# Kernel optimization log

Measured on AMD Instinct MI355X. Metric: run time of the kernel, lower is better.

## Reference

```python
import jax, jax.numpy as jnp
import numpy as np

H, D, E, S_E, P_E, N, B = 16, 48, 768, 384, 128, 768, 1

def _ln(x, g=None, b=None, eps=1e-5):
    mu = jnp.mean(x, axis=-1, keepdims=True)
    var = jnp.var(x, axis=-1, keepdims=True)
    y = (x - mu) * jax.lax.rsqrt(var + eps)
    if g is not None:
        y = y * g
    if b is not None:
        y = y + b
    return y

def setup_inputs() -> dict:
    key = jax.random.key(0)
    ks = jax.random.split(key, 16)
    sc_e = 1.0 / np.sqrt(E)
    sc_s = 1.0 / np.sqrt(S_E)
    sc_p = 1.0 / np.sqrt(P_E)
    return {
        "a": jax.random.normal(ks[0], (B, N, E), jnp.float32),
        "s": jax.random.normal(ks[1], (B, N, S_E), jnp.float32),
        "pair_rep": jax.random.normal(ks[2], (B, N, N, P_E), jnp.float32),
        "beta": jax.random.normal(ks[3], (B, N, N), jnp.float32),
        # AdaLN: sigmoid-gated scale and shift from s
        "w_ada_gamma": jax.random.normal(ks[4], (S_E, E), jnp.float32) * sc_s,
        "w_ada_beta": jax.random.normal(ks[5], (S_E, E), jnp.float32) * sc_s,
        # q/k/v projections, stored as [E, H, D]
        "wq": jax.random.normal(ks[6], (E, H, D), jnp.float32) * sc_e,
        "bq": jnp.zeros((H, D), jnp.float32),
        "wk": jax.random.normal(ks[7], (E, H, D), jnp.float32) * sc_e,
        "wv": jax.random.normal(ks[8], (E, H, D), jnp.float32) * sc_e,
        # pair bias: LayerNorm(P_E) + Linear(P_E -> H, no bias)
        "ln_pair_g": jnp.ones((P_E,), jnp.float32),
        "ln_pair_b": jnp.zeros((P_E,), jnp.float32),
        "w_pair": jax.random.normal(ks[9], (P_E, H), jnp.float32) * sc_p,
        # gate projection [E, H, D], no bias, sigmoid
        "w_gate": jax.random.normal(ks[10], (E, H, D), jnp.float32) * sc_e,
        # output projections
        "w_proj_a": jax.random.normal(ks[11], (E, E), jnp.float32) * sc_e,
        "w_out": jax.random.normal(ks[12], (S_E, E), jnp.float32) * sc_s,
        "b_out": jnp.full((E,), -2.0, jnp.float32),
    }

def reference(a, s, pair_rep, beta, w_ada_gamma, w_ada_beta, wq, bq, wk, wv,
              ln_pair_g, ln_pair_b, w_pair, w_gate, w_proj_a, w_out, b_out):
    # AdaLN: normalize a (no affine); gamma/beta conditioned on normalized s
    a_n = _ln(a)
    s_n = _ln(s)
    gamma = jax.nn.sigmoid(s_n @ w_ada_gamma)
    a_mod = gamma * a_n + s_n @ w_ada_beta            # [B,N,E]

    q = jnp.einsum('bne,ehd->bnhd', a_mod, wq) + bq   # [B,N,H,D]
    k = jnp.einsum('bne,ehd->bnhd', a_mod, wk)
    v = jnp.einsum('bne,ehd->bnhd', a_mod, wv)
    g = jax.nn.sigmoid(jnp.einsum('bne,ehd->bnhd', a_mod, w_gate))

    # per-head pair bias: LN(pair) @ w_pair + beta -> [B,H,N,N]
    b = jnp.einsum('bnmp,ph->bhnm', _ln(pair_rep, ln_pair_g, ln_pair_b), w_pair)
    b = b + beta[:, None, :, :]

    scale = 1.0 / np.sqrt(D)
    logits = jnp.einsum('bnhd,bmhd->bhnm', q, k) * scale + b
    weights = jax.nn.softmax(logits, axis=-1)         # [B,H,N,N]

    attn = jnp.einsum('bhnm,bmhd->bhnd', weights, v)
    attn = attn * jnp.moveaxis(g, -2, -3)             # gate per head
    attn = jnp.moveaxis(attn, -3, -2).reshape(a.shape[0], a.shape[1], H * D)
    out = attn @ w_proj_a                             # [B,N,E]
    out = jax.nn.sigmoid(s @ w_out + b_out) * out
    return out
```

## Files before the change

kernel.cpp:

```cpp
#include <hip/hip_runtime.h>
#include <hip/hip_bf16.h>

typedef __attribute__((ext_vector_type(8))) short short8;
typedef __attribute__((ext_vector_type(8))) unsigned short u16x8;
typedef __attribute__((ext_vector_type(4))) unsigned short u16x4;
typedef __attribute__((ext_vector_type(4))) float f32x4;
typedef __attribute__((ext_vector_type(4))) unsigned u32x4;

#define NTOK 768
#define ED   768
#define SD   384
#define PD   128
#define NH   16
#define DH   48
#define LGS  778

__device__ __forceinline__ unsigned short f2bf(float x) {
  unsigned u = __builtin_bit_cast(unsigned, x);
  u += 0x7FFFu + ((u >> 16) & 1u);
  return (unsigned short)(u >> 16);
}
__device__ __forceinline__ float bf2f(unsigned short b) {
  unsigned u = ((unsigned)b) << 16;
  return __builtin_bit_cast(float, u);
}
__device__ __forceinline__ float sigm(float x) { return 1.0f / (1.0f + __expf(-x)); }

__device__ __forceinline__ unsigned cvtpk(float a, float b) {
  unsigned r;
  asm("v_cvt_pk_bf16_f32 %0, %1, %2" : "=v"(r) : "v"(a), "v"(b));
  return r;
}
__device__ __forceinline__ float lo2f(unsigned p) {
  return __builtin_bit_cast(float, p << 16);
}
__device__ __forceinline__ float hi2f(unsigned p) {
  return __builtin_bit_cast(float, p & 0xFFFF0000u);
}

__device__ __forceinline__ void gl2lds(const unsigned short* g, unsigned short* l) {
  __builtin_amdgcn_global_load_lds(
      (const __attribute__((address_space(1))) unsigned int*)g,
      (__attribute__((address_space(3))) unsigned int*)l, 16, 0, 0);
}

constexpr size_t SZ_SN   = (size_t)NTOK * SD * 2;
constexpr size_t OFF_SNH = 0;
constexpr size_t OFF_SNL = OFF_SNH + SZ_SN;
constexpr size_t OFF_SRH = OFF_SNL + SZ_SN;
constexpr size_t OFF_SRL = OFF_SRH + SZ_SN;
constexpr size_t OFF_GAM = OFF_SRL + SZ_SN;
constexpr size_t OFF_BET = OFF_GAM + 2359296;
constexpr size_t OFF_OG  = OFF_BET + 2359296;
constexpr size_t OFF_AMH = OFF_OG  + 2359296;
constexpr size_t OFF_AML = OFF_AMH + 1179648;
constexpr size_t OFF_QB  = OFF_AML + 1179648;
constexpr size_t OFF_KB  = OFF_QB  + 1179648;
constexpr size_t OFF_VT  = OFF_KB  + 1179648;
constexpr size_t OFF_GBUF= OFF_VT  + 1179648;
constexpr size_t OFF_AGH = OFF_GBUF+ 2359296;
constexpr size_t OFF_AGL = OFF_AGH + 1179648;
constexpr size_t OFF_WSMH= OFF_AGL + 1179648;
constexpr size_t OFF_WSML= OFF_WSMH+ 1769472;
constexpr size_t OFF_WQH = OFF_WSML+ 1769472;
constexpr size_t OFF_WQL = OFF_WQH + 4718592;
constexpr size_t OFF_WPH = OFF_WQL + 4718592;
constexpr size_t OFF_WPL = OFF_WPH + 1179648;
constexpr size_t OFF_GWH = OFF_WPL + 1179648;
constexpr size_t OFF_GWL = OFF_GWH + 4096;
constexpr size_t OFF_SGW = OFF_GWL + 4096;
constexpr size_t OFF_QKL = OFF_SGW + 4096;
constexpr size_t OFF_PB  = OFF_QKL + 37748736;
constexpr size_t WS_NEED = OFF_PB  + 18874368;

__global__ __launch_bounds__(256) void k_wcvt(
    const float* __restrict__ wag, const float* __restrict__ wab, const float* __restrict__ wo,
    const float* __restrict__ wq, const float* __restrict__ wk, const float* __restrict__ wv,
    const float* __restrict__ wg, const float* __restrict__ wp,
    const float* __restrict__ lng, const float* __restrict__ lnb,
    const float* __restrict__ wpair, const float* __restrict__ s,
    unsigned short* __restrict__ wsmh, unsigned short* __restrict__ wsml,
    unsigned short* __restrict__ wqh, unsigned short* __restrict__ wql,
    unsigned short* __restrict__ wph, unsigned short* __restrict__ wpl,
    unsigned short* __restrict__ gwh, unsigned short* __restrict__ gwl,
    float* __restrict__ sgw, float* __restrict__ bw,
    unsigned short* __restrict__ snh, unsigned short* __restrict__ snl,
    unsigned short* __restrict__ srh, unsigned short* __restrict__ srl) {
  const int tid = threadIdx.x;
  if (blockIdx.z == 8) {
    const int gid = blockIdx.y * 24 + blockIdx.x;
    if (gid == 192) {
      if (tid < 128) {
        float g = lng[tid];
        for (int hh = 0; hh < 16; ++hh) {
          float gwv = g * wpair[tid * 16 + hh];
          unsigned short hb = f2bf(gwv);
          gwh[tid * 16 + hh] = hb;
          gwl[tid * 16 + hh] = f2bf(gwv - bf2f(hb));
        }
      }
      if (tid < 16) {
        float sv = 0.f, bb = 0.f;
        for (int p = 0; p < 128; ++p) {
          float w = wpair[p * 16 + tid];
          sv += lng[p] * w;
          bb += lnb[p] * w;
        }
        sgw[tid] = sv;
        bw[tid]  = bb;
      }
      return;
    }
    if (gid > 192) return;
    const int n = gid * 4 + (tid >> 6);
    const int lane = tid & 63;
    const float* row = s + (size_t)n * SD;
    float v[6], sum = 0.f, sq = 0.f;
#pragma unroll
    for (int i = 0; i < 6; ++i) { v[i] = row[lane + 64 * i]; sum += v[i]; sq += v[i] * v[i]; }
#pragma unroll
    for (int off = 1; off < 64; off <<= 1) { sum += __shfl_xor(sum, off); sq += __shfl_xor(sq, off); }
    float mu = sum * (1.f / SD);
    float var = sq * (1.f / SD) - mu * mu;
    float rs = rsqrtf(var + 1e-5f);
#pragma unroll
    for (int i = 0; i < 6; ++i) {
      size_t idx = (size_t)n * SD + lane + 64 * i;
      float x = v[i];
      unsigned short xh = f2bf(x);
      srh[idx] = xh; srl[idx] = f2bf(x - bf2f(xh));
      float y = (x - mu) * rs;
      unsigned short yh = f2bf(y);
      snh[idx] = yh; snl[idx] = f2bf(y - bf2f(yh));
    }
    return;
  }
  const int id = blockIdx.z;
  const float* src; int Ksrc; unsigned short *dh, *dl; int n0; int Kd;
  switch (id) {
    case 0: src = wag; Ksrc = 384; dh = wsmh; dl = wsml; n0 = 0;    Kd = 384; break;
    case 1: src = wab; Ksrc = 384; dh = wsmh; dl = wsml; n0 = 768;  Kd = 384; break;
    case 2: src = wo;  Ksrc = 384; dh = wsmh; dl = wsml; n0 = 1536; Kd = 384; break;
    case 3: src = wq;  Ksrc = 768; dh = wqh;  dl = wql;  n0 = 0;    Kd = 768; break;
    case 4: src = wk;  Ksrc = 768; dh = wqh;  dl = wql;  n0 = 768;  Kd = 768; break;
    case 5: src = wv;  Ksrc = 768; dh = wqh;  dl = wql;  n0 = 1536; Kd = 768; break;
    case 6: src = wg;  Ksrc = 768; dh = wqh;  dl = wql;  n0 = 2304; Kd = 768; break;
    default: src = wp; Ksrc = 768; dh = wph;  dl = wpl;  n0 = 0;    Kd = 768; break;
  }
  const int kt = blockIdx.x, ntile = blockIdx.y;
  if (kt * 32 >= Ksrc) return;
  __shared__ float t[32][33];
  const int r = tid >> 3, c4 = (tid & 7) * 4;
  float4 v = *(const float4*)(src + (size_t)(kt * 32 + r) * 768 + ntile * 32 + c4);
  t[r][c4 + 0] = v.x; t[r][c4 + 1] = v.y; t[r][c4 + 2] = v.z; t[r][c4 + 3] = v.w;
  __syncthreads();
  u16x4 hv, lv;
#pragma unroll
  for (int j = 0; j < 4; ++j) {
    float x = t[c4 + j][r];
    unsigned short hb = f2bf(x);
    hv[j] = hb;
    lv[j] = f2bf(x - bf2f(hb));
  }
  size_t drow = (size_t)(n0 + ntile * 32 + r) * Kd + kt * 32 + c4;
  *(u16x4*)(dh + drow) = hv;
  *(u16x4*)(dl + drow) = lv;
}

__device__ __forceinline__ void mfma_core(
    const unsigned short* __restrict__ Ah, const unsigned short* __restrict__ Al,
    const unsigned short* __restrict__ Bh, const unsigned short* __restrict__ Bl,
    int K, int mBase, int nBase, f32x4 acc[2][2]) {
  __shared__ unsigned short lds[2][4][4096];
  const int tid = threadIdx.x;
  const int w = tid >> 6, lane = tid & 63;
  const int l15 = lane & 15, kg = lane >> 4;
  const int wr = w >> 1, wc = w & 1;

  size_t offA[2], offB[2];
  int ldsw[2];
#pragma unroll
  for (int i = 0; i < 2; ++i) {
    int chunk = w * 128 + i * 64 + lane;
    int row = chunk >> 3;
    int slot = (chunk & 7) ^ (row & 7);
    offA[i] = (size_t)(mBase + row) * K + slot * 8;
    offB[i] = (size_t)(nBase + row) * K + slot * 8;
    ldsw[i] = w * 1024 + i * 512;
  }
  auto stage = [&](int b, int k0) {
#pragma unroll
    for (int i = 0; i < 2; ++i) {
      gl2lds(Ah + offA[i] + k0, &lds[b][0][ldsw[i]]);
      gl2lds(Al + offA[i] + k0, &lds[b][1][ldsw[i]]);
      gl2lds(Bh + offB[i] + k0, &lds[b][2][ldsw[i]]);
      gl2lds(Bl + offB[i] + k0, &lds[b][3][ldsw[i]]);
    }
  };

  stage(0, 0);
  int buf = 0;
  for (int k0 = 64; k0 <= K; k0 += 64) {
    __syncthreads();
    if (k0 < K) stage(buf ^ 1, k0);
#pragma unroll
    for (int kk = 0; kk < 2; ++kk) {
      short8 ah[2], al[2], bh4[2], bl4[2];
#pragma unroll
      for (int mi = 0; mi < 2; ++mi) {
        int row = wr * 32 + mi * 16 + l15;
        int kb = kk * 64 + kg * 16;
        int idx = row * 64 + ((kb ^ ((row & 7) << 4)) >> 1);
        ah[mi] = *(const short8*)&lds[buf][0][idx];
        al[mi] = *(const short8*)&lds[buf][1][idx];
      }
#pragma unroll
      for (int ni = 0; ni < 2; ++ni) {
        int row = wc * 32 + ni * 16 + l15;
        int kb = kk * 64 + kg * 16;
        int idx = row * 64 + ((kb ^ ((row & 7) << 4)) >> 1);
        bh4[ni] = *(const short8*)&lds[buf][2][idx];
        bl4[ni] = *(const short8*)&lds[buf][3][idx];
      }
#pragma unroll
      for (int mi = 0; mi < 2; ++mi)
#pragma unroll
        for (int ni = 0; ni < 2; ++ni) {
          acc[mi][ni] = __builtin_amdgcn_mfma_f32_16x16x32_bf16(ah[mi], bh4[ni], acc[mi][ni], 0, 0, 0);
          acc[mi][ni] = __builtin_amdgcn_mfma_f32_16x16x32_bf16(al[mi], bh4[ni], acc[mi][ni], 0, 0, 0);
          acc[mi][ni] = __builtin_amdgcn_mfma_f32_16x16x32_bf16(ah[mi], bl4[ni], acc[mi][ni], 0, 0, 0);
        }
    }
    buf ^= 1;
  }
}

__global__ __launch_bounds__(256) void k_gemm_small(
    const unsigned short* __restrict__ snh, const unsigned short* __restrict__ snl,
    const unsigned short* __restrict__ srh, const unsigned short* __restrict__ srl,
    const unsigned short* __restrict__ wsmh, const unsigned short* __restrict__ wsml,
    const float* __restrict__ bo,
    float* __restrict__ gaml, float* __restrict__ betl, float* __restrict__ og) {
  const int nt = blockIdx.x, mt = blockIdx.y;
  const unsigned short* Ah = (nt < 24) ? snh : srh;
  const unsigned short* Al = (nt < 24) ? snl : srl;
  f32x4 acc[2][2];
#pragma unroll
  for (int i = 0; i < 2; ++i)
#pragma unroll
    for (int j = 0; j < 2; ++j) acc[i][j] = (f32x4){0.f, 0.f, 0.f, 0.f};
  mfma_core(Ah, Al, wsmh, wsml, SD, mt * 64, nt * 64, acc);
  const int tid = threadIdx.x;
  const int w = tid >> 6, lane = tid & 63;
  const int l15 = lane & 15, kg = lane >> 4;
  const int wr = w >> 1, wc = w & 1;
#pragma unroll
  for (int mi = 0; mi < 2; ++mi)
#pragma unroll
    for (int ni = 0; ni < 2; ++ni) {
      int col = nt * 64 + wc * 32 + ni * 16 + l15;
#pragma unroll
      for (int r = 0; r < 4; ++r) {
        int row = mt * 64 + wr * 32 + mi * 16 + kg * 4 + r;
        float v = acc[mi][ni][r];
        if (col < 768) gaml[(size_t)row * ED + col] = v;
        else if (col < 1536) betl[(size_t)row * ED + col - 768] = v;
        else og[(size_t)row * ED + col - 1536] = sigm(v + bo[col - 1536]);
      }
    }
}

__global__ __launch_bounds__(256) void k_gemm_qkvg(
    const unsigned short* __restrict__ amh, const unsigned short* __restrict__ aml,
    const unsigned short* __restrict__ wqh, const unsigned short* __restrict__ wql,
    const float* __restrict__ bq,
    unsigned short* __restrict__ qb, unsigned short* __restrict__ kb,
    unsigned short* __restrict__ vT, float* __restrict__ gbuf) {
  const int nt = blockIdx.x, mt = blockIdx.y;
  f32x4 acc[2][2];
#pragma unroll
  for (int i = 0; i < 2; ++i)
#pragma unroll
    for (int j = 0; j < 2; ++j) acc[i][j] = (f32x4){0.f, 0.f, 0.f, 0.f};
  mfma_core(amh, aml, wqh, wql, ED, mt * 64, nt * 64, acc);
  const int tid = threadIdx.x;
  const int w = tid >> 6, lane = tid & 63;
  const int l15 = lane & 15, kg = lane >> 4;
  const int wr = w >> 1, wc = w & 1;
  const int sel = nt / 12;
#pragma unroll
  for (int mi = 0; mi < 2; ++mi)
#pragma unroll
    for (int ni = 0; ni < 2; ++ni) {
      int col = nt * 64 + wc * 32 + ni * 16 + l15;
      int c = col - sel * 768;
#pragma unroll
      for (int r = 0; r < 4; ++r) {
        int row = mt * 64 + wr * 32 + mi * 16 + kg * 4 + r;
        float v = acc[mi][ni][r];
        size_t idx = (size_t)row * ED + c;
        if (sel == 0) qb[idx] = f2bf(v + bq[c]);
        else if (sel == 1) kb[idx] = f2bf(v);
        else if (sel == 2) vT[(size_t)c * NTOK + row] = f2bf(v);
        else gbuf[idx] = sigm(v);
      }
    }
}

__global__ __launch_bounds__(256) void k_gemm_proj(
    const unsigned short* __restrict__ agh, const unsigned short* __restrict__ agl,
    const unsigned short* __restrict__ wph, const unsigned short* __restrict__ wpl,
    const float* __restrict__ og, float* __restrict__ out) {
  const int nt = blockIdx.x, mt = blockIdx.y;
  f32x4 acc[2][2];
#pragma unroll
  for (int i = 0; i < 2; ++i)
#pragma unroll
    for (int j = 0; j < 2; ++j) acc[i][j] = (f32x4){0.f, 0.f, 0.f, 0.f};
  mfma_core(agh, agl, wph, wpl, ED, mt * 64, nt * 64, acc);
  const int tid = threadIdx.x;
  const int w = tid >> 6, lane = tid & 63;
  const int l15 = lane & 15, kg = lane >> 4;
  const int wr = w >> 1, wc = w & 1;
#pragma unroll
  for (int mi = 0; mi < 2; ++mi)
#pragma unroll
    for (int ni = 0; ni < 2; ++ni) {
      int col = nt * 64 + wc * 32 + ni * 16 + l15;
#pragma unroll
      for (int r = 0; r < 4; ++r) {
        int row = mt * 64 + wr * 32 + mi * 16 + kg * 4 + r;
        size_t idx = (size_t)row * ED + col;
        out[idx] = acc[mi][ni][r] * og[idx];
      }
    }
}

__global__ __launch_bounds__(256) void k_amod(const float* __restrict__ a,
                                              const float* __restrict__ gamma_lin,
                                              const float* __restrict__ beta_lin,
                                              unsigned short* __restrict__ amh,
                                              unsigned short* __restrict__ aml) {
  __shared__ float red[8];
  const int n = blockIdx.x, tid = threadIdx.x;
  const int lane = tid & 63, wid = tid >> 6;
  const float* row = a + (size_t)n * ED;
  float v[3], sum = 0.f, sq = 0.f;
#pragma unroll
  for (int i = 0; i < 3; ++i) { v[i] = row[tid + 256 * i]; sum += v[i]; sq += v[i] * v[i]; }
#pragma unroll
  for (int off = 1; off < 64; off <<= 1) { sum += __shfl_xor(sum, off); sq += __shfl_xor(sq, off); }
  if (lane == 0) { red[wid] = sum; red[4 + wid] = sq; }
  __syncthreads();
  float S = red[0] + red[1] + red[2] + red[3];
  float Q = red[4] + red[5] + red[6] + red[7];
  float mu = S * (1.f / ED);
  float var = Q * (1.f / ED) - mu * mu;
  float rs = rsqrtf(var + 1e-5f);
#pragma unroll
  for (int i = 0; i < 3; ++i) {
    int e = tid + 256 * i;
    float an = (v[i] - mu) * rs;
    size_t idx = (size_t)n * ED + e;
    float val = sigm(gamma_lin[idx]) * an + beta_lin[idx];
    unsigned short h = f2bf(val);
    amh[idx] = h;
    aml[idx] = f2bf(val - bf2f(h));
  }
}

__global__ __launch_bounds__(256) void k_qkw(const unsigned short* __restrict__ qb,
                                             const unsigned short* __restrict__ kb,
                                             const float* __restrict__ beta,
                                             float* __restrict__ qkl) {
  const int mt = blockIdx.x, ntile = blockIdx.y, h = blockIdx.z;
  __shared__ unsigned short qs[64 * 72];
  __shared__ unsigned short ksm[64 * 72];
  const int tid = threadIdx.x;
  const int n0 = ntile * 64, m0 = mt * 64;
  const u16x8 z = {0, 0, 0, 0, 0, 0, 0, 0};
#pragma unroll
  for (int it = 0; it < 2; ++it) {
    int idx = tid + it * 256;
    int row = idx >> 3, c = idx & 7;
    u16x8 vq = z, vk = z;
    if (c < 6) {
      vq = *(const u16x8*)(qb + (size_t)(n0 + row) * ED + h * DH + c * 8);
      vk = *(const u16x8*)(kb + (size_t)(m0 + row) * ED + h * DH + c * 8);
    }
    *(u16x8*)(qs + row * 72 + c * 8) = vq;
    *(u16x8*)(ksm + row * 72 + c * 8) = vk;
  }
  __syncthreads();
  const int wv = tid >> 6, lane = tid & 63;
  const int l15 = lane & 15, kg = lane >> 4;
  f32x4 acc[4];
#pragma unroll
  for (int ct = 0; ct < 4; ++ct) acc[ct] = (f32x4){0.f, 0.f, 0.f, 0.f};
#pragma unroll
  for (int ks2 = 0; ks2 < 2; ++ks2) {
    short8 av = *(const short8*)(qs + (wv * 16 + l15) * 72 + ks2 * 32 + kg * 8);
#pragma unroll
    for (int ct = 0; ct < 4; ++ct) {
      short8 bv = *(const short8*)(ksm + (ct * 16 + l15) * 72 + ks2 * 32 + kg * 8);
      acc[ct] = __builtin_amdgcn_mfma_f32_16x16x32_bf16(av, bv, acc[ct], 0, 0, 0);
    }
  }
  const float scale = 0.14433756729740643f;
#pragma unroll
  for (int ct = 0; ct < 4; ++ct)
#pragma unroll
    for (int r = 0; r < 4; ++r) {
      int nn = n0 + wv * 16 + kg * 4 + r;
      int mm = m0 + ct * 16 + l15;
      qkl[((size_t)nn * NH + h) * NTOK + mm] =
          fmaf(acc[ct][r], scale, beta[(size_t)nn * NTOK + mm]);
    }
}

__global__ __launch_bounds__(256, 3) void k_pairsm(const float* __restrict__ pair_rep,
                                                   const float* __restrict__ qkl,
                                                   const unsigned short* __restrict__ gw_hi,
                                                   const unsigned short* __restrict__ gw_lo,
                                                   const float* __restrict__ sgw, const float* __restrict__ bw,
                                                   unsigned short* __restrict__ pb) {
  __shared__ float lg[16 * LGS];
  const int n = blockIdx.x;
  const int tid = threadIdx.x;
  const int wv = tid >> 6, lane = tid & 63;
  const int l15 = lane & 15, kg = lane >> 4;

#define LOADCH(X, CH) do {                                                        \
    const float* xp_ = pair_rep + ((size_t)n * NTOK + (CH) * 16 + l15) * PD + kg * 8; \
    _Pragma("unroll")                                                             \
    for (int q_ = 0; q_ < 4; ++q_) {                                              \
      X[q_ * 2]     = *(const float4*)(xp_ + q_ * 32);                            \
      X[q_ * 2 + 1] = *(const float4*)(xp_ + q_ * 32 + 4);                        \
    }                                                                             \
  } while (0)

  float4 Xa[8], Xb[8];
  LOADCH(Xa, wv);
  LOADCH(Xb, wv + 4);

  short8 bh[4], bl[4];
#pragma unroll
  for (int ks = 0; ks < 4; ++ks)
#pragma unroll
    for (int j = 0; j < 8; ++j) {
      int p = ks * 32 + kg * 8 + j;
      bh[ks][j] = (short)gw_hi[p * 16 + l15];
      bl[ks][j] = (short)gw_lo[p * 16 + l15];
    }
  float sgv[4], bwv[4];
#pragma unroll
  for (int r = 0; r < 4; ++r) { sgv[r] = sgw[kg * 4 + r]; bwv[r] = bw[kg * 4 + r]; }

#define PROC(X, CH) do {                                                          \
    float sum_ = 0.f, sq_ = 0.f;                                                  \
    _Pragma("unroll")                                                             \
    for (int q_ = 0; q_ < 8; ++q_) {                                              \
      sum_ += X[q_].x + X[q_].y + X[q_].z + X[q_].w;                              \
      sq_ = fmaf(X[q_].x, X[q_].x, sq_); sq_ = fmaf(X[q_].y, X[q_].y, sq_);       \
      sq_ = fmaf(X[q_].z, X[q_].z, sq_); sq_ = fmaf(X[q_].w, X[q_].w, sq_);       \
    }                                                                             \
    sum_ += __shfl_xor(sum_, 16); sum_ += __shfl_xor(sum_, 32);                   \
    sq_  += __shfl_xor(sq_, 16);  sq_  += __shfl_xor(sq_, 32);                    \
    float mu_ = sum_ * (1.f / 128.f);                                             \
    float rstd_ = rsqrtf(sq_ * (1.f / 128.f) - mu_ * mu_ + 1e-5f);                \
    f32x4 acc_ = {0.f, 0.f, 0.f, 0.f};                                            \
    _Pragma("unroll")                                                             \
    for (int ks_ = 0; ks_ < 4; ++ks_) {                                           \
      float4 u0_ = X[ks_ * 2], u1_ = X[ks_ * 2 + 1];                              \
      unsigned p0_ = cvtpk(u0_.x, u0_.y), p1_ = cvtpk(u0_.z, u0_.w);              \
      unsigned p2_ = cvtpk(u1_.x, u1_.y), p3_ = cvtpk(u1_.z, u1_.w);              \
      float l0_ = u0_.x - lo2f(p0_), l1_ = u0_.y - hi2f(p0_);                     \
      float l2_ = u0_.z - lo2f(p1_), l3_ = u0_.w - hi2f(p1_);                     \
      float l4_ = u1_.x - lo2f(p2_), l5_ = u1_.y - hi2f(p2_);                     \
      float l6_ = u1_.z - lo2f(p3_), l7_ = u1_.w - hi2f(p3_);                     \
      unsigned q0_ = cvtpk(l0_, l1_), q1_ = cvtpk(l2_, l3_);                      \
      unsigned q2_ = cvtpk(l4_, l5_), q3_ = cvtpk(l6_, l7_);                      \
      u32x4 hp_ = {p0_, p1_, p2_, p3_}, lp_ = {q0_, q1_, q2_, q3_};               \
      short8 ah_ = __builtin_bit_cast(short8, hp_);                               \
      short8 al_ = __builtin_bit_cast(short8, lp_);                               \
      acc_ = __builtin_amdgcn_mfma_f32_16x16x32_bf16(bh[ks_], ah_, acc_, 0, 0, 0);\
      acc_ = __builtin_amdgcn_mfma_f32_16x16x32_bf16(bh[ks_], al_, acc_, 0, 0, 0);\
      acc_ = __builtin_amdgcn_mfma_f32_16x16x32_bf16(bl[ks_], ah_, acc_, 0, 0, 0);\
    }                                                                             \
    _Pragma("unroll")                                                             \
    for (int r_ = 0; r_ < 4; ++r_) {                                              \
      float val_ = rstd_ * (acc_[r_] - mu_ * sgv[r_]) + bwv[r_];                  \
      lg[(kg * 4 + r_) * LGS + (CH) * 16 + l15] = val_;                           \
    }                                                                             \
  } while (0)

  PROC(Xa, wv +  0); LOADCH(Xa, wv +  8);
  PROC(Xb, wv +  4); LOADCH(Xb, wv + 12);
  PROC(Xa, wv +  8); LOADCH(Xa, wv + 16);
  PROC(Xb, wv + 12); LOADCH(Xb, wv + 20);
  PROC(Xa, wv + 16); LOADCH(Xa, wv + 24);
  PROC(Xb, wv + 20); LOADCH(Xb, wv + 28);
  PROC(Xa, wv + 24); LOADCH(Xa, wv + 32);
  PROC(Xb, wv + 28); LOADCH(Xb, wv + 36);
  PROC(Xa, wv + 32); LOADCH(Xa, wv + 40);
  PROC(Xb, wv + 36); LOADCH(Xb, wv + 44);
  PROC(Xa, wv + 40);
  PROC(Xb, wv + 44);
#undef LOADCH
#undef PROC
  __syncthreads();

#pragma unroll
  for (int hh = 0; hh < 4; ++hh) {
    int h = wv * 4 + hh;
    const float* qrow = qkl + ((size_t)n * NH + h) * NTOK;
    float x[12];
#pragma unroll
    for (int i = 0; i < 12; ++i) x[i] = lg[h * LGS + lane + 64 * i] + qrow[lane + 64 * i];
    float mx = x[0];
#pragma unroll
    for (int t = 1; t < 12; ++t) mx = fmaxf(mx, x[t]);
#pragma unroll
    for (int off = 1; off < 64; off <<= 1) mx = fmaxf(mx, __shfl_xor(mx, off));
    float e[12], sm = 0.f;
#pragma unroll
    for (int t = 0; t < 12; ++t) { e[t] = __expf(x[t] - mx); sm += e[t]; }
#pragma unroll
    for (int off = 1; off < 64; off <<= 1) sm += __shfl_xor(sm, off);
    float inv = 1.0f / sm;
    unsigned short* dst = pb + ((size_t)h * NTOK + n) * NTOK;
#pragma unroll
    for (int i = 0; i < 12; ++i) dst[lane + 64 * i] = f2bf(e[i] * inv);
  }
}

__global__ __launch_bounds__(256) void k_pv(const unsigned short* __restrict__ wb,
                                            const unsigned short* __restrict__ vT,
                                            const float* __restrict__ gbuf,
                                            unsigned short* __restrict__ agh,
                                            unsigned short* __restrict__ agl) {
  const int ntile = blockIdx.x, h = blockIdx.y;
  const int n0 = ntile * 64;
  __shared__ unsigned short wsm[2][64 * 40];
  __shared__ unsigned short vtm[2][48 * 40];
  const int tid = threadIdx.x;
  const int wv = tid >> 6, lane = tid & 63, l15 = lane & 15, kg = lane >> 4;
  const int srow = tid >> 2, sc = tid & 3;
  const unsigned short* wsrc = wb + ((size_t)h * NTOK + (n0 + srow)) * NTOK + sc * 8;
  const unsigned short* vsrc = (tid < 192)
      ? vT + (size_t)(h * DH + srow) * NTOK + sc * 8 : nullptr;
  f32x4 acc[3];
#pragma unroll
  for (int dt = 0; dt < 3; ++dt) acc[dt] = (f32x4){0.f, 0.f, 0.f, 0.f};

  *(u16x8*)(wsm[0] + srow * 40 + sc * 8) = *(const u16x8*)(wsrc);
  if (tid < 192)
    *(u16x8*)(vtm[0] + srow * 40 + sc * 8) = *(const u16x8*)(vsrc);
  __syncthreads();

  int buf = 0;
  for (int k0 = 0; k0 < NTOK; k0 += 32) {
    if (k0 + 32 < NTOK) {
      *(u16x8*)(wsm[buf ^ 1] + srow * 40 + sc * 8) = *(const u16x8*)(wsrc + k0 + 32);
      if (tid < 192)
        *(u16x8*)(vtm[buf ^ 1] + srow * 40 + sc * 8) = *(const u16x8*)(vsrc + k0 + 32);
    }
    short8 av = *(const short8*)(wsm[buf] + (wv * 16 + l15) * 40 + kg * 8);
#pragma unroll
    for (int dt = 0; dt < 3; ++dt) {
      short8 bv = *(const short8*)(vtm[buf] + (dt * 16 + l15) * 40 + kg * 8);
      acc[dt] = __builtin_amdgcn_mfma_f32_16x16x32_bf16(av, bv, acc[dt], 0, 0, 0);
    }
    __syncthreads();
    buf ^= 1;
  }
#pragma unroll
  for (int dt = 0; dt < 3; ++dt)
#pragma unroll
    for (int r = 0; r < 4; ++r) {
      int nn = n0 + wv * 16 + kg * 4 + r;
      int col = h * DH + dt * 16 + l15;
      size_t idx = (size_t)nn * ED + col;
      float val = acc[dt][r] * gbuf[idx];
      unsigned short hb = f2bf(val);
      agh[idx] = hb;
      agl[idx] = f2bf(val - bf2f(hb));
    }
}

extern "C" void kernel_launch(void* const* d_in, const int* in_sizes, int n_in,
                              void* d_out, int out_size, void* d_ws, size_t ws_size,
                              hipStream_t stream) {
  const float* a    = (const float*)d_in[0];
  const float* s    = (const float*)d_in[1];
  const float* pair = (const float*)d_in[2];
  const float* beta = (const float*)d_in[3];
  const float* wag  = (const float*)d_in[4];
  const float* wab  = (const float*)d_in[5];
  const float* wq   = (const float*)d_in[6];
  const float* bq   = (const float*)d_in[7];
  const float* wk   = (const float*)d_in[8];
  const float* wvp  = (const float*)d_in[9];
  const float* lng  = (const float*)d_in[10];
  const float* lnb  = (const float*)d_in[11];
  const float* wpair= (const float*)d_in[12];
  const float* wg   = (const float*)d_in[13];
  const float* wproj= (const float*)d_in[14];
  const float* wo   = (const float*)d_in[15];
  const float* bo   = (const float*)d_in[16];
  float* out = (float*)d_out;

  if (ws_size < WS_NEED) return;

  char* ws = (char*)d_ws;
  unsigned short* snh  = (unsigned short*)(ws + OFF_SNH);
  unsigned short* snl  = (unsigned short*)(ws + OFF_SNL);
  unsigned short* srh  = (unsigned short*)(ws + OFF_SRH);
  unsigned short* srl  = (unsigned short*)(ws + OFF_SRL);
  float*          gaml = (float*)(ws + OFF_GAM);
  float*          betl = (float*)(ws + OFF_BET);
  float*          og   = (float*)(ws + OFF_OG);
  unsigned short* amh  = (unsigned short*)(ws + OFF_AMH);
  unsigned short* aml  = (unsigned short*)(ws + OFF_AML);
  unsigned short* qb   = (unsigned short*)(ws + OFF_QB);
  unsigned short* kb   = (unsigned short*)(ws + OFF_KB);
  unsigned short* vT   = (unsigned short*)(ws + OFF_VT);
  float*          gbuf = (float*)(ws + OFF_GBUF);
  unsigned short* agh  = (unsigned short*)(ws + OFF_AGH);
  unsigned short* agl  = (unsigned short*)(ws + OFF_AGL);
  unsigned short* wsmh = (unsigned short*)(ws + OFF_WSMH);
  unsigned short* wsml = (unsigned short*)(ws + OFF_WSML);
  unsigned short* wqh  = (unsigned short*)(ws + OFF_WQH);
  unsigned short* wql  = (unsigned short*)(ws + OFF_WQL);
  unsigned short* wph  = (unsigned short*)(ws + OFF_WPH);
  unsigned short* wpl  = (unsigned short*)(ws + OFF_WPL);
  unsigned short* gwh  = (unsigned short*)(ws + OFF_GWH);
  unsigned short* gwl  = (unsigned short*)(ws + OFF_GWL);
  float*          sgw  = (float*)(ws + OFF_SGW);
  float*          bw   = sgw + 16;
  float*          qkl  = (float*)(ws + OFF_QKL);
  unsigned short* pb   = (unsigned short*)(ws + OFF_PB);

  hipLaunchKernelGGL(k_wcvt, dim3(24, 24, 9), dim3(256), 0, stream,
                     wag, wab, wo, wq, wk, wvp, wg, wproj, lng, lnb, wpair, s,
                     wsmh, wsml, wqh, wql, wph, wpl, gwh, gwl, sgw, bw,
                     snh, snl, srh, srl);
  hipLaunchKernelGGL(k_gemm_small, dim3(36, 12), dim3(256), 0, stream,
                     snh, snl, srh, srl, wsmh, wsml, bo, gaml, betl, og);
  hipLaunchKernelGGL(k_amod, dim3(768), dim3(256), 0, stream, a, gaml, betl, amh, aml);
  hipLaunchKernelGGL(k_gemm_qkvg, dim3(48, 12), dim3(256), 0, stream,
                     amh, aml, wqh, wql, bq, qb, kb, vT, gbuf);
  hipLaunchKernelGGL(k_qkw, dim3(12, 12, 16), dim3(256), 0, stream, qb, kb, beta, qkl);
  hipLaunchKernelGGL(k_pairsm, dim3(768), dim3(256), 0, stream,
                     pair, qkl, gwh, gwl, sgw, bw, pb);
  hipLaunchKernelGGL(k_pv, dim3(12, 16), dim3(256), 0, stream, pb, vT, gbuf, agh, agl);
  hipLaunchKernelGGL(k_gemm_proj, dim3(12, 12), dim3(256), 0, stream,
                     agh, agl, wph, wpl, og, out);
}
```

Baseline: 172.1 us.

## Offload pair-bias LN+projection for first rows into QKVG GEMM launch

Adds 192 extra blocks to the QKVG GEMM grid that compute the layer-normed pair bias for the first 192 query rows and write it to a new global buffer. The pair-softmax kernel then reads the precomputed bias for those rows instead of streaming pair_rep, and computes it inline only for the remaining rows. The aim is to fill idle compute units during the small GEMM and shorten the memory-bound pair kernel. The cost is an extra global round trip of fp32 bias and a larger, more divergent GEMM launch.

```diff
diff --git a/kernel.cpp b/kernel.cpp
--- a/kernel.cpp
+++ b/kernel.cpp
@@ -14,6 +14,7 @@
 #define NH   16
 #define DH   48
 #define LGS  778
+#define NRIDE 192
 
 __device__ __forceinline__ unsigned short f2bf(float x) {
   unsigned u = __builtin_bit_cast(unsigned, x);
@@ -71,7 +72,8 @@
 constexpr size_t OFF_SGW = OFF_GWL + 4096;
 constexpr size_t OFF_QKL = OFF_SGW + 4096;
 constexpr size_t OFF_PB  = OFF_QKL + 37748736;
-constexpr size_t WS_NEED = OFF_PB  + 18874368;
+constexpr size_t OFF_BB  = OFF_PB  + 18874368;
+constexpr size_t WS_NEED = OFF_BB  + 9437184;
 
 __global__ __launch_bounds__(256) void k_wcvt(
     const float* __restrict__ wag, const float* __restrict__ wab, const float* __restrict__ wo,
@@ -167,6 +169,95 @@
   *(u16x4*)(dl + drow) = lv;
 }
 
+__device__ __forceinline__ void pair_bias_rows_to_global(
+    int n, const float* __restrict__ pair_rep,
+    const unsigned short* __restrict__ gw_hi, const unsigned short* __restrict__ gw_lo,
+    const float* __restrict__ sgw, const float* __restrict__ bw,
+    float* __restrict__ bb) {
+  const int tid = threadIdx.x;
+  const int wv = tid >> 6, lane = tid & 63;
+  const int l15 = lane & 15, kg = lane >> 4;
+
+#define LOADCH2(X, CH) do {                                                       \
+    const float* xp_ = pair_rep + ((size_t)n * NTOK + (CH) * 16 + l15) * PD + kg * 8; \
+    _Pragma("unroll")                                                             \
+    for (int q_ = 0; q_ < 4; ++q_) {                                              \
+      X[q_ * 2]     = *(const float4*)(xp_ + q_ * 32);                            \
+      X[q_ * 2 + 1] = *(const float4*)(xp_ + q_ * 32 + 4);                        \
+    }                                                                             \
+  } while (0)
+
+  float4 Xa[8], Xb[8];
+  LOADCH2(Xa, wv);
+  LOADCH2(Xb, wv + 4);
+
+  short8 bh[4], bl[4];
+#pragma unroll
+  for (int ks = 0; ks < 4; ++ks)
+#pragma unroll
+    for (int j = 0; j < 8; ++j) {
+      int p = ks * 32 + kg * 8 + j;
+      bh[ks][j] = (short)gw_hi[p * 16 + l15];
+      bl[ks][j] = (short)gw_lo[p * 16 + l15];
+    }
+  float sgv[4], bwv[4];
+#pragma unroll
+  for (int r = 0; r < 4; ++r) { sgv[r] = sgw[kg * 4 + r]; bwv[r] = bw[kg * 4 + r]; }
+
+#define PROC2(X, CH) do {                                                         \
+    float sum_ = 0.f, sq_ = 0.f;                                                  \
+    _Pragma("unroll")                                                             \
+    for (int q_ = 0; q_ < 8; ++q_) {                                              \
+      sum_ += X[q_].x + X[q_].y + X[q_].z + X[q_].w;                              \
+      sq_ = fmaf(X[q_].x, X[q_].x, sq_); sq_ = fmaf(X[q_].y, X[q_].y, sq_);       \
+      sq_ = fmaf(X[q_].z, X[q_].z, sq_); sq_ = fmaf(X[q_].w, X[q_].w, sq_);       \
+    }                                                                             \
+    sum_ += __shfl_xor(sum_, 16); sum_ += __shfl_xor(sum_, 32);                   \
+    sq_  += __shfl_xor(sq_, 16);  sq_  += __shfl_xor(sq_, 32);                    \
+    float mu_ = sum_ * (1.f / 128.f);                                             \
+    float rstd_ = rsqrtf(sq_ * (1.f / 128.f) - mu_ * mu_ + 1e-5f);                \
+    f32x4 acc_ = {0.f, 0.f, 0.f, 0.f};                                            \
+    _Pragma("unroll")                                                             \
+    for (int ks_ = 0; ks_ < 4; ++ks_) {                                           \
+      float4 u0_ = X[ks_ * 2], u1_ = X[ks_ * 2 + 1];                              \
+      unsigned p0_ = cvtpk(u0_.x, u0_.y), p1_ = cvtpk(u0_.z, u0_.w);              \
+      unsigned p2_ = cvtpk(u1_.x, u1_.y), p3_ = cvtpk(u1_.z, u1_.w);              \
+      float l0_ = u0_.x - lo2f(p0_), l1_ = u0_.y - hi2f(p0_);                     \
+      float l2_ = u0_.z - lo2f(p1_), l3_ = u0_.w - hi2f(p1_);                     \
+      float l4_ = u1_.x - lo2f(p2_), l5_ = u1_.y - hi2f(p2_);                     \
+      float l6_ = u1_.z - lo2f(p3_), l7_ = u1_.w - hi2f(p3_);                     \
+      unsigned q0_ = cvtpk(l0_, l1_), q1_ = cvtpk(l2_, l3_);                      \
+      unsigned q2_ = cvtpk(l4_, l5_), q3_ = cvtpk(l6_, l7_);                      \
+      u32x4 hp_ = {p0_, p1_, p2_, p3_}, lp_ = {q0_, q1_, q2_, q3_};               \
+      short8 ah_ = __builtin_bit_cast(short8, hp_);                               \
+      short8 al_ = __builtin_bit_cast(short8, lp_);                               \
+      acc_ = __builtin_amdgcn_mfma_f32_16x16x32_bf16(bh[ks_], ah_, acc_, 0, 0, 0);\
+      acc_ = __builtin_amdgcn_mfma_f32_16x16x32_bf16(bh[ks_], al_, acc_, 0, 0, 0);\
+      acc_ = __builtin_amdgcn_mfma_f32_16x16x32_bf16(bl[ks_], ah_, acc_, 0, 0, 0);\
+    }                                                                             \
+    _Pragma("unroll")                                                             \
+    for (int r_ = 0; r_ < 4; ++r_) {                                              \
+      float val_ = rstd_ * (acc_[r_] - mu_ * sgv[r_]) + bwv[r_];                  \
+      bb[(size_t)n * (NH * NTOK) + (kg * 4 + r_) * NTOK + (CH) * 16 + l15] = val_;\
+    }                                                                             \
+  } while (0)
+
+  PROC2(Xa, wv +  0); LOADCH2(Xa, wv +  8);
+  PROC2(Xb, wv +  4); LOADCH2(Xb, wv + 12);
+  PROC2(Xa, wv +  8); LOADCH2(Xa, wv + 16);
+  PROC2(Xb, wv + 12); LOADCH2(Xb, wv + 20);
+  PROC2(Xa, wv + 16); LOADCH2(Xa, wv + 24);
+  PROC2(Xb, wv + 20); LOADCH2(Xb, wv + 28);
+  PROC2(Xa, wv + 24); LOADCH2(Xa, wv + 32);
+  PROC2(Xb, wv + 28); LOADCH2(Xb, wv + 36);
+  PROC2(Xa, wv + 32); LOADCH2(Xa, wv + 40);
+  PROC2(Xb, wv + 36); LOADCH2(Xb, wv + 44);
+  PROC2(Xa, wv + 40);
+  PROC2(Xb, wv + 44);
+#undef LOADCH2
+#undef PROC2
+}
+
 __device__ __forceinline__ void mfma_core(
     const unsigned short* __restrict__ Ah, const unsigned short* __restrict__ Al,
     const unsigned short* __restrict__ Bh, const unsigned short* __restrict__ Bl,
@@ -274,9 +365,17 @@
     const unsigned short* __restrict__ amh, const unsigned short* __restrict__ aml,
     const unsigned short* __restrict__ wqh, const unsigned short* __restrict__ wql,
     const float* __restrict__ bq,
+    const float* __restrict__ pair_rep,
+    const unsigned short* __restrict__ gwh, const unsigned short* __restrict__ gwl,
+    const float* __restrict__ sgw, const float* __restrict__ bw,
+    float* __restrict__ biasBuf,
     unsigned short* __restrict__ qb, unsigned short* __restrict__ kb,
     unsigned short* __restrict__ vT, float* __restrict__ gbuf) {
   const int nt = blockIdx.x, mt = blockIdx.y;
+  if (mt >= 12) {
+    pair_bias_rows_to_global((mt - 12) * 48 + nt, pair_rep, gwh, gwl, sgw, bw, biasBuf);
+    return;
+  }
   f32x4 acc[2][2];
 #pragma unroll
   for (int i = 0; i < 2; ++i)
@@ -420,6 +519,7 @@
 
 __global__ __launch_bounds__(256, 3) void k_pairsm(const float* __restrict__ pair_rep,
                                                    const float* __restrict__ qkl,
+                                                   const float* __restrict__ biasBuf,
                                                    const unsigned short* __restrict__ gw_hi,
                                                    const unsigned short* __restrict__ gw_lo,
                                                    const float* __restrict__ sgw, const float* __restrict__ bw,
@@ -429,7 +529,9 @@
   const int tid = threadIdx.x;
   const int wv = tid >> 6, lane = tid & 63;
   const int l15 = lane & 15, kg = lane >> 4;
-
+  const bool buffered = (n < NRIDE);
+
+  if (!buffered) {
 #define LOADCH(X, CH) do {                                                        \
     const float* xp_ = pair_rep + ((size_t)n * NTOK + (CH) * 16 + l15) * PD + kg * 8; \
     _Pragma("unroll")                                                             \
@@ -439,22 +541,22 @@
     }                                                                             \
   } while (0)
 
-  float4 Xa[8], Xb[8];
-  LOADCH(Xa, wv);
-  LOADCH(Xb, wv + 4);
-
-  short8 bh[4], bl[4];
-#pragma unroll
-  for (int ks = 0; ks < 4; ++ks)
-#pragma unroll
-    for (int j = 0; j < 8; ++j) {
-      int p = ks * 32 + kg * 8 + j;
-      bh[ks][j] = (short)gw_hi[p * 16 + l15];
-      bl[ks][j] = (short)gw_lo[p * 16 + l15];
-    }
-  float sgv[4], bwv[4];
-#pragma unroll
-  for (int r = 0; r < 4; ++r) { sgv[r] = sgw[kg * 4 + r]; bwv[r] = bw[kg * 4 + r]; }
+    float4 Xa[8], Xb[8];
+    LOADCH(Xa, wv);
+    LOADCH(Xb, wv + 4);
+
+    short8 bh[4], bl[4];
+#pragma unroll
+    for (int ks = 0; ks < 4; ++ks)
+#pragma unroll
+      for (int j = 0; j < 8; ++j) {
+        int p = ks * 32 + kg * 8 + j;
+        bh[ks][j] = (short)gw_hi[p * 16 + l15];
+        bl[ks][j] = (short)gw_lo[p * 16 + l15];
+      }
+    float sgv[4], bwv[4];
+#pragma unroll
+    for (int r = 0; r < 4; ++r) { sgv[r] = sgw[kg * 4 + r]; bwv[r] = bw[kg * 4 + r]; }
 
 #define PROC(X, CH) do {                                                          \
     float sum_ = 0.f, sq_ = 0.f;                                                  \
@@ -494,29 +596,36 @@
     }                                                                             \
   } while (0)
 
-  PROC(Xa, wv +  0); LOADCH(Xa, wv +  8);
-  PROC(Xb, wv +  4); LOADCH(Xb, wv + 12);
-  PROC(Xa, wv +  8); LOADCH(Xa, wv + 16);
-  PROC(Xb, wv + 12); LOADCH(Xb, wv + 20);
-  PROC(Xa, wv + 16); LOADCH(Xa, wv + 24);
-  PROC(Xb, wv + 20); LOADCH(Xb, wv + 28);
-  PROC(Xa, wv + 24); LOADCH(Xa, wv + 32);
-  PROC(Xb, wv + 28); LOADCH(Xb, wv + 36);
-  PROC(Xa, wv + 32); LOADCH(Xa, wv + 40);
-  PROC(Xb, wv + 36); LOADCH(Xb, wv + 44);
-  PROC(Xa, wv + 40);
-  PROC(Xb, wv + 44);
+    PROC(Xa, wv +  0); LOADCH(Xa, wv +  8);
+    PROC(Xb, wv +  4); LOADCH(Xb, wv + 12);
+    PROC(Xa, wv +  8); LOADCH(Xa, wv + 16);
+    PROC(Xb, wv + 12); LOADCH(Xb, wv + 20);
+    PROC(Xa, wv + 16); LOADCH(Xa, wv + 24);
+    PROC(Xb, wv + 20); LOADCH(Xb, wv + 28);
+    PROC(Xa, wv + 24); LOADCH(Xa, wv + 32);
+    PROC(Xb, wv + 28); LOADCH(Xb, wv + 36);
+    PROC(Xa, wv + 32); LOADCH(Xa, wv + 40);
+    PROC(Xb, wv + 36); LOADCH(Xb, wv + 44);
+    PROC(Xa, wv + 40);
+    PROC(Xb, wv + 44);
 #undef LOADCH
 #undef PROC
-  __syncthreads();
+    __syncthreads();
+  }
 
 #pragma unroll
   for (int hh = 0; hh < 4; ++hh) {
     int h = wv * 4 + hh;
     const float* qrow = qkl + ((size_t)n * NH + h) * NTOK;
+    const float* brow = biasBuf + ((size_t)n * NH + h) * NTOK;
     float x[12];
-#pragma unroll
-    for (int i = 0; i < 12; ++i) x[i] = lg[h * LGS + lane + 64 * i] + qrow[lane + 64 * i];
+    if (buffered) {
+#pragma unroll
+      for (int i = 0; i < 12; ++i) x[i] = brow[lane + 64 * i] + qrow[lane + 64 * i];
+    } else {
+#pragma unroll
+      for (int i = 0; i < 12; ++i) x[i] = lg[h * LGS + lane + 64 * i] + qrow[lane + 64 * i];
+    }
     float mx = x[0];
 #pragma unroll
     for (int t = 1; t < 12; ++t) mx = fmaxf(mx, x[t]);
@@ -640,6 +749,7 @@
   float*          bw   = sgw + 16;
   float*          qkl  = (float*)(ws + OFF_QKL);
   unsigned short* pb   = (unsigned short*)(ws + OFF_PB);
+  float*          bb   = (float*)(ws + OFF_BB);
 
   hipLaunchKernelGGL(k_wcvt, dim3(24, 24, 9), dim3(256), 0, stream,
                      wag, wab, wo, wq, wk, wvp, wg, wproj, lng, lnb, wpair, s,
@@ -648,11 +758,12 @@
   hipLaunchKernelGGL(k_gemm_small, dim3(36, 12), dim3(256), 0, stream,
                      snh, snl, srh, srl, wsmh, wsml, bo, gaml, betl, og);
   hipLaunchKernelGGL(k_amod, dim3(768), dim3(256), 0, stream, a, gaml, betl, amh, aml);
-  hipLaunchKernelGGL(k_gemm_qkvg, dim3(48, 12), dim3(256), 0, stream,
-                     amh, aml, wqh, wql, bq, qb, kb, vT, gbuf);
+  hipLaunchKernelGGL(k_gemm_qkvg, dim3(48, 16), dim3(256), 0, stream,
+                     amh, aml, wqh, wql, bq, pair, gwh, gwl, sgw, bw, bb,
+                     qb, kb, vT, gbuf);
   hipLaunchKernelGGL(k_qkw, dim3(12, 12, 16), dim3(256), 0, stream, qb, kb, beta, qkl);
   hipLaunchKernelGGL(k_pairsm, dim3(768), dim3(256), 0, stream,
-                     pair, qkl, gwh, gwl, sgw, bw, pb);
+                     pair, qkl, bb, gwh, gwl, sgw, bw, pb);
   hipLaunchKernelGGL(k_pv, dim3(12, 16), dim3(256), 0, stream, pb, vT, gbuf, agh, agl);
   hipLaunchKernelGGL(k_gemm_proj, dim3(12, 12), dim3(256), 0, stream,
                      agh, agl, wph, wpl, og, out);
```

Result: slower. 187.9 us (+9.2%).
